# Optimization experiments

Measured on AMD Instinct MI355X. Metric: run time of the kernel, lower is better.

The kernel has to match this reference:

```python
import jax, jax.numpy as jnp
import numpy as np

N, D, H, E = 4096, 256, 8, 131072
HD = D // H
EPS = 1e-5


def layernorm(x, g, b):
    mu = jnp.mean(x, axis=-1, keepdims=True)
    var = jnp.mean((x - mu) ** 2, axis=-1, keepdims=True)
    return (x - mu) * jax.lax.rsqrt(var + EPS) * g + b


def setup_inputs() -> dict:
    key = jax.random.key(0)
    ks = jax.random.split(key, 20)
    s = 1.0 / np.sqrt(D)
    x = jax.random.normal(ks[0], (N, D), jnp.float32)
    adj = jax.random.uniform(ks[1], (N, N)) < 0.01
    adj_mask = adj | jnp.eye(N, dtype=bool)  # self-loops keep softmax rows finite
    edge_index = jax.random.randint(ks[2], (2, E), 0, N, dtype=jnp.int64)
    edge_attr = jax.random.normal(ks[3], (E, D), jnp.float32)
    p = {
        'wq': jax.random.normal(ks[4], (D, D)) * s, 'bq': jnp.zeros((D,)),
        'wk': jax.random.normal(ks[5], (D, D)) * s, 'bk': jnp.zeros((D,)),
        'wv': jax.random.normal(ks[6], (D, D)) * s, 'bv': jnp.zeros((D,)),
        'wo': jax.random.normal(ks[7], (D, D)) * s, 'bo': jnp.zeros((D,)),
        'we': jax.random.normal(ks[8], (D, H)) * s, 'be': jnp.zeros((H,)),
        'w1': jax.random.normal(ks[9], (D, 4 * D)) * s, 'b1': jnp.zeros((4 * D,)),
        'w2': jax.random.normal(ks[10], (4 * D, D)) * (1.0 / np.sqrt(4 * D)), 'b2': jnp.zeros((D,)),
        'g1': jnp.ones((D,)), 'beta1': jnp.zeros((D,)),
        'g2': jnp.ones((D,)), 'beta2': jnp.zeros((D,)),
    }
    return dict(x=x, adj_mask=adj_mask, edge_index=edge_index, edge_attr=edge_attr, **p)


def reference(x, adj_mask, edge_index, edge_attr, wq, bq, wk, bk, wv, bv, wo, bo,
              we, be, w1, b1, w2, b2, g1, beta1, g2, beta2):
    n = x.shape[0]
    Q = (x @ wq + bq).reshape(n, H, HD)
    K = (x @ wk + bk).reshape(n, H, HD)
    V = (x @ wv + bv).reshape(n, H, HD)
    scores = jnp.einsum('nhd,mhd->nmh', Q, K) / np.sqrt(HD)  # [N,N,H]
    edge_bias = edge_attr @ we + be                          # [E,H]
    scores = scores.at[edge_index[0], edge_index[1]].add(edge_bias)
    s = jnp.transpose(scores, (0, 2, 1))                     # [N,H,N]
    s = jnp.where(adj_mask[:, None, :], s, -jnp.inf)
    attn = jax.nn.softmax(s, axis=-1)                        # dropout eval-mode no-op
    ctx = jnp.einsum('nhm,mhd->nhd', attn, V).reshape(n, D)
    attn_out = ctx @ wo + bo
    x1 = layernorm(x + attn_out, g1, beta1)
    ff = jax.nn.gelu(x1 @ w1 + b1, approximate=False) @ w2 + b2
    return layernorm(x1 + ff, g2, beta2)
```

## Files before the change

### kernel.cpp

```cpp
#include <hip/hip_runtime.h>
#include <math.h>

#define NN   4096
#define DD   256
#define HH   8
#define HD   32
#define DFF  1024
#define QKVW 768
#define AC   128
#define EC   128
#define SCPAD 129
#define QSP  36
#define NPB  2

typedef unsigned short ushort_t;
typedef __attribute__((ext_vector_type(8))) short short8;
typedef __attribute__((ext_vector_type(4))) float f32x4;

__device__ __forceinline__ float bf2f(unsigned short u){
  union { unsigned int i; float f; } v; v.i = ((unsigned int)u) << 16; return v.f;
}
__device__ __forceinline__ unsigned short f2bf(float f){
  union { float f; unsigned int i; } v; v.f = f;
  unsigned int x = v.i;
  return (unsigned short)((x + 0x7FFFu + ((x >> 16) & 1u)) >> 16);
}
__device__ __forceinline__ float ldf(const void* p, size_t i, int isbf){
  return isbf ? bf2f(((const ushort_t*)p)[i]) : ((const float*)p)[i];
}
__device__ __forceinline__ ushort_t ldb16(const void* p, size_t i, int isbf){
  return isbf ? ((const ushort_t*)p)[i] : f2bf(((const float*)p)[i]);
}

__global__ void k_detect(const int* __restrict__ adj32, const int* __restrict__ ei32,
                         const unsigned int* __restrict__ g1w, int* __restrict__ flags,
                         int* __restrict__ counts, int* __restrict__ cursor){
  __shared__ int c0s, c1s;
  int t = threadIdx.x;
  if (t == 0) { c0s = 0; c1s = 0; }
  __syncthreads();
  int c0 = 0, c1 = 0;
  for (int i = t; i < 960; i += 256) if (adj32[(size_t)i * 4097] != 0) c0++;
  for (int i = t; i < 2048; i += 256) if (ei32[2*i + 1] != 0) c1++;
  atomicAdd(&c0s, c0); atomicAdd(&c1s, c1);
  for (int i = t; i < NN; i += 256) { counts[i] = 0; cursor[i] = 0; }
  __syncthreads();
  if (t == 0) {
    flags[0] = (c0s == 960) ? 1 : 0;
    flags[1] = (c1s > 100) ? 1 : 0;
    flags[2] = (g1w[0] == 0x3F803F80u) ? 1 : 0;
  }
}

#define NX    (NN * DD)
#define NWE   (DD * HH)
#define TPREP 768
#define NCSR  NN
__global__ __launch_bounds__(256) void k_prep(
    const void* __restrict__ adj, int* __restrict__ alist, int* __restrict__ acnt,
    const void* __restrict__ x, const void* __restrict__ wq, const void* __restrict__ wk,
    const void* __restrict__ wv, const void* __restrict__ wo, const void* __restrict__ w1,
    const void* __restrict__ w2, const void* __restrict__ we,
    const void* __restrict__ bq, const void* __restrict__ bk, const void* __restrict__ bv,
    const void* __restrict__ bo, const void* __restrict__ be, const void* __restrict__ b1,
    const void* __restrict__ b2, const void* __restrict__ g1, const void* __restrict__ be1,
    const void* __restrict__ g2, const void* __restrict__ be2,
    const int* __restrict__ ei, const int* __restrict__ flags,
    ushort_t* __restrict__ xb,
    ushort_t* __restrict__ wqkvT, ushort_t* __restrict__ woT,
    ushort_t* __restrict__ w1T, ushort_t* __restrict__ w2T,
    float* __restrict__ wef, float* __restrict__ bqkvf,
    float* __restrict__ bof, float* __restrict__ bef,
    float* __restrict__ b1f, float* __restrict__ b2f,
    float* __restrict__ g1f, float* __restrict__ be1f,
    float* __restrict__ g2f, float* __restrict__ be2f,
    int* __restrict__ counts, int E, int TOT)
{
  const int isbf = flags[2];
  const int t = threadIdx.x;
  if (blockIdx.x < NCSR) {
    __shared__ int cntS;
    __shared__ int actS[AC];
    const int n = blockIdx.x;
    if (t == 0) cntS = 0;
    __syncthreads();
    if (flags[0]) {
      const uint4* arow = (const uint4*)((const int*)adj + (size_t)n * NN);
      #pragma unroll
      for (int i = 0; i < 4; i++) {
        uint4 v = arow[t + 256 * i];
        int c0 = 4 * (t + 256 * i);
        if (v.x) { int p = atomicAdd(&cntS, 1); if (p < AC) actS[p] = c0; }
        if (v.y) { int p = atomicAdd(&cntS, 1); if (p < AC) actS[p] = c0 + 1; }
        if (v.z) { int p = atomicAdd(&cntS, 1); if (p < AC) actS[p] = c0 + 2; }
        if (v.w) { int p = atomicAdd(&cntS, 1); if (p < AC) actS[p] = c0 + 3; }
      }
    } else {
      const uint4* arow = (const uint4*)((const unsigned char*)adj + (size_t)n * NN);
      uint4 v = arow[t];
      unsigned int wsv[4] = {v.x, v.y, v.z, v.w};
      #pragma unroll
      for (int q = 0; q < 4; q++) {
        unsigned int u = wsv[q];
        int c0 = 16 * t + 4 * q;
        if (u & 0x000000FFu) { int p = atomicAdd(&cntS, 1); if (p < AC) actS[p] = c0; }
        if (u & 0x0000FF00u) { int p = atomicAdd(&cntS, 1); if (p < AC) actS[p] = c0 + 1; }
        if (u & 0x00FF0000u) { int p = atomicAdd(&cntS, 1); if (p < AC) actS[p] = c0 + 2; }
        if (u & 0xFF000000u) { int p = atomicAdd(&cntS, 1); if (p < AC) actS[p] = c0 + 3; }
      }
    }
    __syncthreads();
    int m = cntS; if (m > AC) m = AC;
    if (t == 0) acnt[n] = m;
    for (int j = t; j < m; j += 256) alist[(size_t)n * AC + j] = actS[j];
    return;
  }
  if (blockIdx.x < NCSR + TPREP) {
    __shared__ ushort_t tile[32][36];
    int b = blockIdx.x - NCSR;
    const void* src; ushort_t* dst; int R, C, ti;
    if (b < 64)       { src = wq; dst = wqkvT;              R = 256;  C = 256;  ti = b; }
    else if (b < 128) { src = wk; dst = wqkvT + 256 * 256;  R = 256;  C = 256;  ti = b - 64; }
    else if (b < 192) { src = wv; dst = wqkvT + 512 * 256;  R = 256;  C = 256;  ti = b - 128; }
    else if (b < 256) { src = wo; dst = woT;                R = 256;  C = 256;  ti = b - 192; }
    else if (b < 512) { src = w1; dst = w1T;                R = 256;  C = 1024; ti = b - 256; }
    else              { src = w2; dst = w2T;                R = 1024; C = 256;  ti = b - 512; }
    int tiles_c = C >> 5;
    int tr = ti / tiles_c, tc = ti - tr * tiles_c;
    int lr = t >> 3, lc0 = (t & 7) << 2;
    size_t sbase = (size_t)(tr * 32 + lr) * C + tc * 32 + lc0;
    if (isbf) {
      const ushort_t* s16 = (const ushort_t*)src + sbase;
      tile[lr][lc0+0] = s16[0]; tile[lr][lc0+1] = s16[1];
      tile[lr][lc0+2] = s16[2]; tile[lr][lc0+3] = s16[3];
    } else {
      const float4* sf = (const float4*)((const float*)src + sbase);
      float4 v = *sf;
      tile[lr][lc0+0] = f2bf(v.x); tile[lr][lc0+1] = f2bf(v.y);
      tile[lr][lc0+2] = f2bf(v.z); tile[lr][lc0+3] = f2bf(v.w);
    }
    __syncthreads();
    int i = t >> 3, j0 = (t & 7) << 2;
    ushort_t* dp = dst + (size_t)(tc * 32 + i) * R + tr * 32 + j0;
    ushort_t o0 = tile[j0][i], o1 = tile[j0+1][i], o2 = tile[j0+2][i], o3 = tile[j0+3][i];
    dp[0] = o0; dp[1] = o1; dp[2] = o2; dp[3] = o3;
    return;
  }
  const int ei32 = flags[1];
  const int stride = (gridDim.x - NCSR - TPREP) * 256;
  for (int i = (blockIdx.x - NCSR - TPREP) * 256 + t; i < TOT; i += stride) {
    int r = i;
    if (r < NX) { xb[r] = ldb16(x, r, isbf); continue; }
    r -= NX;
    if (r < E) {
      int src = ei32 ? ei[r] : ei[2 * r];
      if ((unsigned)src < (unsigned)NN) atomicAdd(&counts[src], 1);
      continue;
    }
    r -= E;
    if (r < NWE) { wef[r] = ldf(we, r, isbf); continue; }
    r -= NWE;
    if (r < QKVW) {
      const void* bs = (r < 256) ? bq : (r < 512) ? bk : bv;
      bqkvf[r] = ldf(bs, r & 255, isbf);
      continue;
    }
    r -= QKVW;
    if (r < DD)  { bof[r] = ldf(bo, r, isbf); continue; }   r -= DD;
    if (r < HH)  { bef[r] = ldf(be, r, isbf); continue; }   r -= HH;
    if (r < DFF) { b1f[r] = ldf(b1, r, isbf); continue; }   r -= DFF;
    if (r < DD)  { b2f[r] = ldf(b2, r, isbf); continue; }   r -= DD;
    if (r < DD)  { g1f[r] = ldf(g1, r, isbf); continue; }   r -= DD;
    if (r < DD)  { be1f[r] = ldf(be1, r, isbf); continue; } r -= DD;
    if (r < DD)  { g2f[r] = ldf(g2, r, isbf); continue; }   r -= DD;
    if (r < DD)  { be2f[r] = ldf(be2, r, isbf); }
  }
}

#define LDK 72
__global__ __launch_bounds__(256) void k_gemm(
    const ushort_t* __restrict__ A, const ushort_t* __restrict__ Bt,
    const float* __restrict__ bias, void* __restrict__ C,
    int M, int Nn, int K, int act, int mode,
    float* __restrict__ qf, ushort_t* __restrict__ kbuf, ushort_t* __restrict__ vbuf)
{
  __shared__ ushort_t As[64 * LDK];
  __shared__ ushort_t Bs[64 * LDK];
  const int t = threadIdx.x;
  const int wave = t >> 6, lane = t & 63;
  const int l15 = lane & 15, quad = lane >> 4;
  const int wr = wave >> 1, wc = wave & 1;
  const int bm0 = blockIdx.y * 64, bn0 = blockIdx.x * 64;

  const int arow = t >> 2, akg = (t & 3) << 4;

  f32x4 acc[2][2] = {};

  const ushort_t* ap = A  + (size_t)(bm0 + arow) * K + akg;
  const ushort_t* bp = Bt + (size_t)(bn0 + arow) * K + akg;
  uint4 a0 = *(const uint4*)ap;
  uint4 a1 = *(const uint4*)(ap + 8);
  uint4 b0 = *(const uint4*)bp;
  uint4 b1 = *(const uint4*)(bp + 8);

  for (int k0 = 0; k0 < K; k0 += 64) {
    __syncthreads();
    *(uint4*)(&As[arow * LDK + akg]) = a0;
    *(uint4*)(&As[arow * LDK + akg + 8]) = a1;
    *(uint4*)(&Bs[arow * LDK + akg]) = b0;
    *(uint4*)(&Bs[arow * LDK + akg + 8]) = b1;
    __syncthreads();
    if (k0 + 64 < K) {
      a0 = *(const uint4*)(ap + k0 + 64);
      a1 = *(const uint4*)(ap + k0 + 64 + 8);
      b0 = *(const uint4*)(bp + k0 + 64);
      b1 = *(const uint4*)(bp + k0 + 64 + 8);
    }
    #pragma unroll
    for (int kk = 0; kk < 2; kk++) {
      short8 af[2], bf[2];
      #pragma unroll
      for (int fr = 0; fr < 2; fr++)
        af[fr] = *(const short8*)(&As[(wr * 32 + fr * 16 + l15) * LDK + kk * 32 + quad * 8]);
      #pragma unroll
      for (int fc = 0; fc < 2; fc++)
        bf[fc] = *(const short8*)(&Bs[(wc * 32 + fc * 16 + l15) * LDK + kk * 32 + quad * 8]);
      #pragma unroll
      for (int fr = 0; fr < 2; fr++)
        #pragma unroll
        for (int fc = 0; fc < 2; fc++)
          acc[fr][fc] = __builtin_amdgcn_mfma_f32_16x16x32_bf16(af[fr], bf[fc], acc[fr][fc], 0, 0, 0);
    }
  }

  #pragma unroll
  for (int fr = 0; fr < 2; fr++) {
    #pragma unroll
    for (int fc = 0; fc < 2; fc++) {
      int gn = bn0 + wc * 32 + fc * 16 + l15;
      float bcol = bias[gn];
      #pragma unroll
      for (int r = 0; r < 4; r++) {
        int gm = bm0 + wr * 32 + fr * 16 + quad * 4 + r;
        float v = acc[fr][fc][r] + bcol;
        if (act) v = 0.5f * v * (1.0f + erff(v * 0.70710678118654752f));
        if (mode == 2) {
          if (gn < 256)      qf[(size_t)gm * 256 + gn] = v;
          else if (gn < 512) kbuf[(size_t)gm * 256 + (gn - 256)] = f2bf(v);
          else               vbuf[(size_t)gm * 256 + (gn - 512)] = f2bf(v);
        } else {
          ((ushort_t*)C)[(size_t)gm * Nn + gn] = f2bf(v);
        }
      }
    }
  }
}

__global__ __launch_bounds__(256) void k_mid(
    const ushort_t* __restrict__ A, const ushort_t* __restrict__ Bt,
    const float* __restrict__ bias,
    float* __restrict__ qf, ushort_t* __restrict__ kbuf, ushort_t* __restrict__ vbuf,
    const void* __restrict__ ea, const float* __restrict__ wef,
    const float* __restrict__ bef, float* __restrict__ sbias,
    int E, const int* __restrict__ flags,
    const int* __restrict__ ei, const int* __restrict__ off,
    int* __restrict__ cursor, int* __restrict__ sdst, int* __restrict__ seid)
{
  __shared__ __align__(16) char smem[64 * LDK * 2 * 2];
  const int t = threadIdx.x;
  if (blockIdx.x < 768) {
    ushort_t* As = (ushort_t*)smem;
    ushort_t* Bs = As + 64 * LDK;
    const int wave = t >> 6, lane = t & 63;
    const int l15 = lane & 15, quad = lane >> 4;
    const int wr = wave >> 1, wc = wave & 1;
    const int bn0 = (blockIdx.x % 12) * 64, bm0 = (blockIdx.x / 12) * 64;
    const int arow = t >> 2, akg = (t & 3) << 4;
    const int K = DD;

    f32x4 acc[2][2] = {};

    const ushort_t* ap = A  + (size_t)(bm0 + arow) * K + akg;
    const ushort_t* bp = Bt + (size_t)(bn0 + arow) * K + akg;
    uint4 a0 = *(const uint4*)ap;
    uint4 a1 = *(const uint4*)(ap + 8);
    uint4 b0 = *(const uint4*)bp;
    uint4 b1 = *(const uint4*)(bp + 8);

    for (int k0 = 0; k0 < K; k0 += 64) {
      __syncthreads();
      *(uint4*)(&As[arow * LDK + akg]) = a0;
      *(uint4*)(&As[arow * LDK + akg + 8]) = a1;
      *(uint4*)(&Bs[arow * LDK + akg]) = b0;
      *(uint4*)(&Bs[arow * LDK + akg + 8]) = b1;
      __syncthreads();
      if (k0 + 64 < K) {
        a0 = *(const uint4*)(ap + k0 + 64);
        a1 = *(const uint4*)(ap + k0 + 64 + 8);
        b0 = *(const uint4*)(bp + k0 + 64);
        b1 = *(const uint4*)(bp + k0 + 64 + 8);
      }
      #pragma unroll
      for (int kk = 0; kk < 2; kk++) {
        short8 af[2], bf[2];
        #pragma unroll
        for (int fr = 0; fr < 2; fr++)
          af[fr] = *(const short8*)(&As[(wr * 32 + fr * 16 + l15) * LDK + kk * 32 + quad * 8]);
        #pragma unroll
        for (int fc = 0; fc < 2; fc++)
          bf[fc] = *(const short8*)(&Bs[(wc * 32 + fc * 16 + l15) * LDK + kk * 32 + quad * 8]);
        #pragma unroll
        for (int fr = 0; fr < 2; fr++)
          #pragma unroll
          for (int fc = 0; fc < 2; fc++)
            acc[fr][fc] = __builtin_amdgcn_mfma_f32_16x16x32_bf16(af[fr], bf[fc], acc[fr][fc], 0, 0, 0);
      }
    }

    #pragma unroll
    for (int fr = 0; fr < 2; fr++) {
      #pragma unroll
      for (int fc = 0; fc < 2; fc++) {
        int gn = bn0 + wc * 32 + fc * 16 + l15;
        float bcol = bias[gn];
        #pragma unroll
        for (int r = 0; r < 4; r++) {
          int gm = bm0 + wr * 32 + fr * 16 + quad * 4 + r;
          float v = acc[fr][fc][r] + bcol;
          if (gn < 256)      qf[(size_t)gm * 256 + gn] = v;
          else if (gn < 512) kbuf[(size_t)gm * 256 + (gn - 256)] = f2bf(v);
          else               vbuf[(size_t)gm * 256 + (gn - 512)] = f2bf(v);
        }
      }
    }
    return;
  }
  float* wel = (float*)smem;
  const int b = blockIdx.x - 768;
  #pragma unroll
  for (int j = 0; j < 8; j++) wel[j * DD + t] = wef[t * 8 + j];
  const int isbf = flags[2];
  if (t < 32) {
    int i = b * 32 + t;
    if (i < E) {
      int src, dst;
      if (flags[1]) { src = ei[i];     dst = ei[E + i]; }
      else          { src = ei[2 * i]; dst = ei[2 * (E + i)]; }
      if ((unsigned)src < (unsigned)NN) {
        if ((unsigned)dst >= (unsigned)NN) dst = 0;
        int pos = off[src] + atomicAdd(&cursor[src], 1);
        sdst[pos] = dst; seid[pos] = i;
      }
    }
  }
  __syncthreads();
  int idx = b * 256 + t;
  int e = idx >> 3, p = idx & 7;
  float acc[8] = {};
  if (e < E) {
    if (isbf) {
      const uint4* base = (const uint4*)((const ushort_t*)ea + (size_t)e * DD);
      #pragma unroll
      for (int q = 0; q < 4; q++) {
        uint4 u = base[q * 8 + p];
        int dbase = 64 * q + 8 * p;
        float f[8];
        union { unsigned int i; float f; } cv;
        cv.i = u.x << 16; f[0] = cv.f; cv.i = u.x & 0xFFFF0000u; f[1] = cv.f;
        cv.i = u.y << 16; f[2] = cv.f; cv.i = u.y & 0xFFFF0000u; f[3] = cv.f;
        cv.i = u.z << 16; f[4] = cv.f; cv.i = u.z & 0xFFFF0000u; f[5] = cv.f;
        cv.i = u.w << 16; f[6] = cv.f; cv.i = u.w & 0xFFFF0000u; f[7] = cv.f;
        #pragma unroll
        for (int j = 0; j < 8; j++)
          #pragma unroll
          for (int h = 0; h < 8; h++)
            acc[h] = fmaf(f[j], wel[h * DD + dbase + j], acc[h]);
      }
    } else {
      const float4* base = (const float4*)((const float*)ea + (size_t)e * DD);
      #pragma unroll
      for (int q = 0; q < 8; q++) {
        float4 u = base[q * 8 + p];
        int dbase = 32 * q + 4 * p;
        #pragma unroll
        for (int h = 0; h < 8; h++) {
          acc[h] = fmaf(u.x, wel[h * DD + dbase + 0], acc[h]);
          acc[h] = fmaf(u.y, wel[h * DD + dbase + 1], acc[h]);
          acc[h] = fmaf(u.z, wel[h * DD + dbase + 2], acc[h]);
          acc[h] = fmaf(u.w, wel[h * DD + dbase + 3], acc[h]);
        }
      }
    }
  }
  #pragma unroll
  for (int h = 0; h < 8; h++) {
    acc[h] += __shfl_xor(acc[h], 1, 8);
    acc[h] += __shfl_xor(acc[h], 2, 8);
    acc[h] += __shfl_xor(acc[h], 4, 8);
  }
  if (e < E) sbias[(size_t)e * 8 + p] = acc[p] + bef[p];
}

__global__ __launch_bounds__(512) void k_gemmln(
    const ushort_t* __restrict__ A, const ushort_t* __restrict__ Bt,
    const float* __restrict__ bias, const void* __restrict__ res, int res_raw,
    void* __restrict__ outf, ushort_t* __restrict__ outb,
    const float* __restrict__ g, const float* __restrict__ beta,
    int final_mode, const int* __restrict__ flags, int K)
{
  __shared__ ushort_t As[16 * LDK];
  __shared__ ushort_t Bs[256 * LDK];
  __shared__ float p1[16][8];
  __shared__ float p2[16][8];
  const int t = threadIdx.x;
  const int wave = t >> 6, lane = t & 63;
  const int l15 = lane & 15, quad = lane >> 4;
  const int bm0 = blockIdx.x * 16;

  const int arow = t >> 3, akg = (t & 7) << 3;
  const int brow = t >> 1, bkg = (t & 1) << 5;

  f32x4 acc[2] = {};

  const ushort_t* ap = A + (size_t)(bm0 + arow) * K + akg;
  const ushort_t* bp = Bt + (size_t)brow * K + bkg;
  uint4 a0{};
  if (t < 128) a0 = *(const uint4*)ap;
  uint4 b0 = *(const uint4*)bp;
  uint4 b1 = *(const uint4*)(bp + 8);
  uint4 b2 = *(const uint4*)(bp + 16);
  uint4 b3 = *(const uint4*)(bp + 24);

  for (int k0 = 0; k0 < K; k0 += 64) {
    __syncthreads();
    if (t < 128) *(uint4*)(&As[arow * LDK + akg]) = a0;
    *(uint4*)(&Bs[brow * LDK + bkg])      = b0;
    *(uint4*)(&Bs[brow * LDK + bkg + 8])  = b1;
    *(uint4*)(&Bs[brow * LDK + bkg + 16]) = b2;
    *(uint4*)(&Bs[brow * LDK + bkg + 24]) = b3;
    __syncthreads();
    if (k0 + 64 < K) {
      if (t < 128) a0 = *(const uint4*)(ap + k0 + 64);
      b0 = *(const uint4*)(bp + k0 + 64);
      b1 = *(const uint4*)(bp + k0 + 64 + 8);
      b2 = *(const uint4*)(bp + k0 + 64 + 16);
      b3 = *(const uint4*)(bp + k0 + 64 + 24);
    }
    #pragma unroll
    for (int kk = 0; kk < 2; kk++) {
      short8 af  = *(const short8*)(&As[l15 * LDK + kk * 32 + quad * 8]);
      short8 bf0 = *(const short8*)(&Bs[(wave * 32 +      l15) * LDK + kk * 32 + quad * 8]);
      short8 bf1 = *(const short8*)(&Bs[(wave * 32 + 16 + l15) * LDK + kk * 32 + quad * 8]);
      acc[0] = __builtin_amdgcn_mfma_f32_16x16x32_bf16(af, bf0, acc[0], 0, 0, 0);
      acc[1] = __builtin_amdgcn_mfma_f32_16x16x32_bf16(af, bf1, acc[1], 0, 0, 0);
    }
  }

  const int isbf = flags[2];
  float v[2][4];
  #pragma unroll
  for (int fc = 0; fc < 2; fc++) {
    int gn = wave * 32 + fc * 16 + l15;
    float bc = bias[gn];
    #pragma unroll
    for (int r = 0; r < 4; r++) {
      int gm = bm0 + quad * 4 + r;
      float rv = res_raw ? ldf(res, (size_t)gm * DD + gn, isbf)
                         : ((const float*)res)[(size_t)gm * DD + gn];
      v[fc][r] = acc[fc][r] + bc + rv;
    }
  }
  float s1[4];
  #pragma unroll
  for (int r = 0; r < 4; r++) {
    s1[r] = v[0][r] + v[1][r];
    #pragma unroll
    for (int o = 1; o < 16; o <<= 1) s1[r] += __shfl_xor(s1[r], o, 64);
  }
  if (l15 == 0) {
    #pragma unroll
    for (int r = 0; r < 4; r++) p1[quad * 4 + r][wave] = s1[r];
  }
  __syncthreads();
  float mu[4];
  #pragma unroll
  for (int r = 0; r < 4; r++) {
    float m = 0.f;
    #pragma unroll
    for (int w = 0; w < 8; w++) m += p1[quad * 4 + r][w];
    mu[r] = m * (1.0f / 256.0f);
  }
  float s2[4];
  #pragma unroll
  for (int r = 0; r < 4; r++) {
    float d0 = v[0][r] - mu[r], d1 = v[1][r] - mu[r];
    s2[r] = d0 * d0 + d1 * d1;
    #pragma unroll
    for (int o = 1; o < 16; o <<= 1) s2[r] += __shfl_xor(s2[r], o, 64);
  }
  if (l15 == 0) {
    #pragma unroll
    for (int r = 0; r < 4; r++) p2[quad * 4 + r][wave] = s2[r];
  }
  __syncthreads();
  float rs[4];
  #pragma unroll
  for (int r = 0; r < 4; r++) {
    float q = 0.f;
    #pragma unroll
    for (int w = 0; w < 8; w++) q += p2[quad * 4 + r][w];
    rs[r] = rsqrtf(q * (1.0f / 256.0f) + 1e-5f);
  }
  #pragma unroll
  for (int fc = 0; fc < 2; fc++) {
    int gn = wave * 32 + fc * 16 + l15;
    float gv = g[gn], bv = beta[gn];
    #pragma unroll
    for (int r = 0; r < 4; r++) {
      int gm = bm0 + quad * 4 + r;
      float res_v = (v[fc][r] - mu[r]) * rs[r] * gv + bv;
      if (outb) {
        ((float*)outf)[(size_t)gm * DD + gn] = res_v;
        outb[(size_t)gm * DD + gn] = f2bf(res_v);
      } else {
        if (final_mode && isbf)
          ((ushort_t*)outf)[(size_t)gm * DD + gn] = f2bf(res_v);
        else
          ((float*)outf)[(size_t)gm * DD + gn] = res_v;
      }
    }
  }
}

__global__ __launch_bounds__(256) void k_scan(const int* __restrict__ counts,
                                              int* __restrict__ off){
  __shared__ int wsum[4];
  const int t = threadIdx.x, lid = t & 63, wid = t >> 6;
  int loc[16]; int s = 0;
  #pragma unroll
  for (int j = 0; j < 16; j++) { loc[j] = counts[t * 16 + j]; s += loc[j]; }
  const int tot = s;
  #pragma unroll
  for (int o = 1; o < 64; o <<= 1) {
    int u = __shfl_up(s, o, 64);
    if (lid >= o) s += u;
  }
  if (lid == 63) wsum[wid] = s;
  __syncthreads();
  int pre = 0;
  #pragma unroll
  for (int w = 0; w < 4; w++) if (w < wid) pre += wsum[w];
  int run = pre + s - tot;
  if (t == 0) off[0] = 0;
  #pragma unroll
  for (int j = 0; j < 16; j++) { run += loc[j]; off[t * 16 + j + 1] = run; }
}

__global__ __launch_bounds__(256) void k_attn(
    const float* __restrict__ qf, const ushort_t* __restrict__ kb,
    const ushort_t* __restrict__ vb,
    const int* __restrict__ alist, const int* __restrict__ acnt,
    const int* __restrict__ off, const int* __restrict__ sdst,
    const int* __restrict__ seid, const float* __restrict__ sbias,
    ushort_t* __restrict__ ctxb)
{
  __shared__ float qs[NPB][HH * QSP];
  __shared__ int   act[NPB][AC];
  __shared__ float sc[NPB][HH][SCPAD];
  __shared__ int   edst[NPB][EC];
  __shared__ float ivs[NPB][HH];

  const int t = threadIdx.x;
  const int n0 = blockIdx.x * NPB;

  int na[NPB], cn[NPB], st[NPB];
  #pragma unroll
  for (int s = 0; s < NPB; s++) {
    int n = n0 + s;
    qs[s][(t >> 5) * QSP + (t & 31)] = qf[(size_t)n * DD + t];
    na[s] = min(acnt[n], AC);
    st[s] = off[n];
    int c = off[n + 1] - st[s];
    cn[s] = c < 0 ? 0 : (c > EC ? EC : c);
    for (int j = t; j < na[s]; j += 256) act[s][j] = alist[(size_t)n * AC + j];
    for (int j = t; j < cn[s]; j += 256) edst[s][j] = sdst[st[s] + j];
  }
  __syncthreads();

  #pragma unroll
  for (int s = 0; s < NPB; s++) {
    for (int item = t; item < na[s] * HH; item += 256) {
      int idx = item >> 3, h = item & 7;
      int m = act[s][idx];
      const uint4* kr = (const uint4*)(kb + (size_t)m * DD + h * HD);
      const float* qh = qs[s] + h * QSP;
      float a = 0.f;
      #pragma unroll
      for (int q4 = 0; q4 < 4; q4++) {
        uint4 u = kr[q4];
        int b = q4 * 8;
        union { unsigned int i; float f; } cv;
        cv.i = u.x << 16;         a = fmaf(cv.f, qh[b+0], a);
        cv.i = u.x & 0xFFFF0000u; a = fmaf(cv.f, qh[b+1], a);
        cv.i = u.y << 16;         a = fmaf(cv.f, qh[b+2], a);
        cv.i = u.y & 0xFFFF0000u; a = fmaf(cv.f, qh[b+3], a);
        cv.i = u.z << 16;         a = fmaf(cv.f, qh[b+4], a);
        cv.i = u.z & 0xFFFF0000u; a = fmaf(cv.f, qh[b+5], a);
        cv.i = u.w << 16;         a = fmaf(cv.f, qh[b+6], a);
        cv.i = u.w & 0xFFFF0000u; a = fmaf(cv.f, qh[b+7], a);
      }
      sc[s][h][idx] = a * 0.17677669529663687f;
    }
  }
  __syncthreads();

  #pragma unroll
  for (int s = 0; s < NPB; s++) {
    for (int item = t; item < cn[s] * HH; item += 256) {
      int j = item >> 3, h = item & 7;
      int sid = seid[st[s] + j];
      int dst = edst[s][j];
      int pos = -1;
      for (int i = 0; i < na[s]; i++) if (act[s][i] == dst) { pos = i; break; }
      if (pos >= 0) atomicAdd(&sc[s][h][pos], sbias[(size_t)sid * 8 + h]);
    }
  }
  __syncthreads();

  #pragma unroll
  for (int s = 0; s < NPB; s++) {
    const int h = t >> 5, l = t & 31;
    float lm = -1e30f;
    for (int i = l; i < na[s]; i += 32) lm = fmaxf(lm, sc[s][h][i]);
    #pragma unroll
    for (int o = 16; o > 0; o >>= 1) lm = fmaxf(lm, __shfl_down(lm, o, 32));
    lm = __shfl(lm, 0, 32);
    float ls = 0.f;
    for (int i = l; i < na[s]; i += 32) {
      float e = __expf(sc[s][h][i] - lm);
      sc[s][h][i] = e;
      ls += e;
    }
    #pragma unroll
    for (int o = 16; o > 0; o >>= 1) ls += __shfl_down(ls, o, 32);
    if (l == 0) ivs[s][h] = 1.0f / ls;
  }
  __syncthreads();

  {
    const int s_ = t >> 7, h = (t >> 4) & 7, dp = t & 15;
    const int n_a = s_ ? na[1] : na[0];
    const ushort_t* vcol = vb + h * HD + 2 * dp;
    const float* scp = sc[s_][h];
    float a0 = 0.f, a1 = 0.f;
    int i = 0;
    for (; i + 8 <= n_a; i += 8) {
      int mm[8]; unsigned int vv[8];
      #pragma unroll
      for (int u = 0; u < 8; u++) mm[u] = act[s_][i + u];
      #pragma unroll
      for (int u = 0; u < 8; u++) vv[u] = *(const unsigned int*)(vcol + (size_t)mm[u] * DD);
      #pragma unroll
      for (int u = 0; u < 8; u++) {
        float p = scp[i + u];
        a0 = fmaf(p, bf2f((ushort_t)(vv[u] & 0xFFFFu)), a0);
        a1 = fmaf(p, bf2f((ushort_t)(vv[u] >> 16)), a1);
      }
    }
    for (; i < n_a; i++) {
      unsigned int v = *(const unsigned int*)(vcol + (size_t)act[s_][i] * DD);
      float p = scp[i];
      a0 = fmaf(p, bf2f((ushort_t)(v & 0xFFFFu)), a0);
      a1 = fmaf(p, bf2f((ushort_t)(v >> 16)), a1);
    }
    float iv = ivs[s_][h];
    unsigned int ob = ((unsigned int)f2bf(a1 * iv) << 16) | (unsigned int)f2bf(a0 * iv);
    *(unsigned int*)(ctxb + (size_t)(n0 + s_) * DD + h * HD + 2 * dp) = ob;
  }
}

extern "C" void kernel_launch(void* const* d_in, const int* in_sizes, int n_in,
                              void* d_out, int out_size, void* d_ws, size_t ws_size,
                              hipStream_t stream)
{
  const void* x   = d_in[0];
  const void* adj = d_in[1];
  const int*  ei  = (const int*)d_in[2];
  const void* ea  = d_in[3];
  const void* wq  = d_in[4];  const void* bq  = d_in[5];
  const void* wk  = d_in[6];  const void* bk  = d_in[7];
  const void* wv  = d_in[8];  const void* bv  = d_in[9];
  const void* wo  = d_in[10]; const void* bo  = d_in[11];
  const void* we  = d_in[12]; const void* be  = d_in[13];
  const void* w1  = d_in[14]; const void* b1  = d_in[15];
  const void* w2  = d_in[16]; const void* b2  = d_in[17];
  const void* g1  = d_in[18]; const void* be1 = d_in[19];
  const void* g2  = d_in[20]; const void* be2 = d_in[21];
  const int E = in_sizes[2] / 2;

  char* w = (char*)d_ws;
  size_t o = 0;
  auto carve = [&](size_t bytes) -> void* {
    void* p = w + o; o = (o + bytes + 255) & ~(size_t)255; return p;
  };
  ushort_t* xb    = (ushort_t*)carve((size_t)NN * DD * 2);
  float*    qfb   = (float*)   carve((size_t)NN * DD * 4);
  ushort_t* kbuf  = (ushort_t*)carve((size_t)NN * DD * 2);
  ushort_t* vbuf  = (ushort_t*)carve((size_t)NN * DD * 2);
  ushort_t* wqkvT = (ushort_t*)carve((size_t)QKVW * DD * 2);
  float*    bqkvf = (float*)   carve(QKVW * 4);
  ushort_t* woT   = (ushort_t*)carve((size_t)DD * DD * 2);
  ushort_t* w1T   = (ushort_t*)carve((size_t)DFF * DD * 2);
  ushort_t* w2T   = (ushort_t*)carve((size_t)DD * DFF * 2);
  float*    wef   = (float*)   carve((size_t)DD * HH * 4);
  float*    bof   = (float*)   carve(DD * 4);
  float*    bef   = (float*)   carve(HH * 4);
  float*    b1f   = (float*)   carve(DFF * 4);
  float*    b2f   = (float*)   carve(DD * 4);
  float*    g1f   = (float*)   carve(DD * 4);
  float*    be1f  = (float*)   carve(DD * 4);
  float*    g2f   = (float*)   carve(DD * 4);
  float*    be2f  = (float*)   carve(DD * 4);
  int*      counts = (int*)carve((size_t)NN * 4);
  int*      cursor = (int*)carve((size_t)NN * 4);
  int*      off    = (int*)carve((size_t)(NN + 1) * 4);
  int*      sdst   = (int*)carve((size_t)E * 4);
  int*      seid   = (int*)carve((size_t)E * 4);
  float*    sbias  = (float*)carve((size_t)E * HH * 4);
  int*      alist  = (int*)carve((size_t)NN * AC * 4);
  int*      acnt   = (int*)carve((size_t)NN * 4);
  ushort_t* ctxb     = (ushort_t*)carve((size_t)NN * DD * 2);
  float*    x1f      = (float*)   carve((size_t)NN * DD * 4);
  ushort_t* x1b      = (ushort_t*)carve((size_t)NN * DD * 2);
  ushort_t* hbufb    = (ushort_t*)carve((size_t)NN * DFF * 2);
  int*      flags    = (int*)carve(4 * 4);

  k_detect<<<1, 256, 0, stream>>>((const int*)adj, ei, (const unsigned int*)g1,
                                  flags, counts, cursor);

  const int TOT = NX + E + NWE + QKVW + DD + HH + DFF + DD + DD + DD + DD + DD;
  k_prep<<<NCSR + TPREP + 1280, 256, 0, stream>>>(
      adj, alist, acnt,
      x, wq, wk, wv, wo, w1, w2, we, bq, bk, bv, bo, be, b1, b2,
      g1, be1, g2, be2, ei, flags,
      xb, wqkvT, woT, w1T, w2T, wef, bqkvf,
      bof, bef, b1f, b2f, g1f, be1f, g2f, be2f, counts, E, TOT);

  k_scan<<<1, 256, 0, stream>>>(counts, off);

  int ebb = (E * 8 + 255) / 256;
  k_mid<<<768 + ebb, 256, 0, stream>>>(
      xb, wqkvT, bqkvf, qfb, kbuf, vbuf,
      ea, wef, bef, sbias, E, flags, ei, off, cursor, sdst, seid);

  k_attn<<<NN / NPB, 256, 0, stream>>>(qfb, kbuf, vbuf, alist, acnt, off, sdst,
                                       seid, sbias, ctxb);

  k_gemmln<<<NN / 16, 512, 0, stream>>>(
      ctxb, woT, bof, x, 1, x1f, x1b, g1f, be1f, 0, flags, DD);

  k_gemm<<<dim3(DFF / 64, NN / 64), 256, 0, stream>>>(
      x1b, w1T, b1f, hbufb, NN, DFF, DD, 1, 1, nullptr, nullptr, nullptr);

  k_gemmln<<<NN / 16, 512, 0, stream>>>(
      hbufb, w2T, b2f, x1f, 0, d_out, nullptr, g2f, be2f, 1, flags, DFF);
}
```

Measured before the change: 400.3 us.

## Precompute edge positions in CSR build, process four nodes per attention block

The linear search that maps each edge's destination to its slot in the node's active-neighbour list now runs once in the CSR-building stage of k_mid, which stores that slot index in place of the destination. k_attn reads the slot and edge id directly, so it no longer repeats the search for every head. k_attn also handles four nodes per block instead of two, and each thread accumulates four V columns with 64-bit loads instead of two with 32-bit loads. This adds a serial global-memory search per edge inside k_mid and more shared memory per attention block, which may reduce occupancy.

```diff
diff --git a/kernel.cpp b/kernel.cpp
--- a/kernel.cpp
+++ b/kernel.cpp
@@ -11,7 +11,7 @@
 #define EC   128
 #define SCPAD 129
 #define QSP  36
-#define NPB  2
+#define NPB  4
 
 typedef unsigned short ushort_t;
 typedef __attribute__((ext_vector_type(8))) short short8;
@@ -264,7 +264,8 @@
     const float* __restrict__ bef, float* __restrict__ sbias,
     int E, const int* __restrict__ flags,
     const int* __restrict__ ei, const int* __restrict__ off,
-    int* __restrict__ cursor, int* __restrict__ sdst, int* __restrict__ seid)
+    int* __restrict__ cursor, int* __restrict__ sdst, int* __restrict__ seid,
+    const int* __restrict__ alist, const int* __restrict__ acnt)
 {
   __shared__ __align__(16) char smem[64 * LDK * 2 * 2];
   const int t = threadIdx.x;
@@ -349,7 +350,11 @@
       if ((unsigned)src < (unsigned)NN) {
         if ((unsigned)dst >= (unsigned)NN) dst = 0;
         int pos = off[src] + atomicAdd(&cursor[src], 1);
-        sdst[pos] = dst; seid[pos] = i;
+        int na_s = min(acnt[src], AC);
+        const int* ap_ = alist + (size_t)src * AC;
+        int p = -1;
+        for (int q = 0; q < na_s; q++) if (ap_[q] == dst) { p = q; break; }
+        sdst[pos] = p; seid[pos] = i;
       }
     }
   }
@@ -560,14 +565,15 @@
     const float* __restrict__ qf, const ushort_t* __restrict__ kb,
     const ushort_t* __restrict__ vb,
     const int* __restrict__ alist, const int* __restrict__ acnt,
-    const int* __restrict__ off, const int* __restrict__ sdst,
+    const int* __restrict__ off, const int* __restrict__ spos,
     const int* __restrict__ seid, const float* __restrict__ sbias,
     ushort_t* __restrict__ ctxb)
 {
   __shared__ float qs[NPB][HH * QSP];
   __shared__ int   act[NPB][AC];
   __shared__ float sc[NPB][HH][SCPAD];
-  __shared__ int   edst[NPB][EC];
+  __shared__ int   eposS[NPB][EC];
+  __shared__ int   eidS[NPB][EC];
   __shared__ float ivs[NPB][HH];
 
   const int t = threadIdx.x;
@@ -583,7 +589,10 @@
     int c = off[n + 1] - st[s];
     cn[s] = c < 0 ? 0 : (c > EC ? EC : c);
     for (int j = t; j < na[s]; j += 256) act[s][j] = alist[(size_t)n * AC + j];
-    for (int j = t; j < cn[s]; j += 256) edst[s][j] = sdst[st[s] + j];
+    for (int j = t; j < cn[s]; j += 256) {
+      eposS[s][j] = spos[st[s] + j];
+      eidS[s][j]  = seid[st[s] + j];
+    }
   }
   __syncthreads();
 
@@ -618,11 +627,9 @@
   for (int s = 0; s < NPB; s++) {
     for (int item = t; item < cn[s] * HH; item += 256) {
       int j = item >> 3, h = item & 7;
-      int sid = seid[st[s] + j];
-      int dst = edst[s][j];
-      int pos = -1;
-      for (int i = 0; i < na[s]; i++) if (act[s][i] == dst) { pos = i; break; }
-      if (pos >= 0) atomicAdd(&sc[s][h][pos], sbias[(size_t)sid * 8 + h]);
+      int pos = eposS[s][j];
+      if (pos >= 0)
+        atomicAdd(&sc[s][h][pos], sbias[(size_t)eidS[s][j] * 8 + h]);
     }
   }
   __syncthreads();
@@ -648,34 +655,41 @@
   __syncthreads();
 
   {
-    const int s_ = t >> 7, h = (t >> 4) & 7, dp = t & 15;
-    const int n_a = s_ ? na[1] : na[0];
-    const ushort_t* vcol = vb + h * HD + 2 * dp;
+    const int s_ = t >> 6, h = (t >> 3) & 7, d4 = t & 7;
+    const int n_a = na[s_];
+    const ushort_t* vcol = vb + h * HD + 4 * d4;
     const float* scp = sc[s_][h];
-    float a0 = 0.f, a1 = 0.f;
+    float a0 = 0.f, a1 = 0.f, a2 = 0.f, a3 = 0.f;
     int i = 0;
     for (; i + 8 <= n_a; i += 8) {
-      int mm[8]; unsigned int vv[8];
+      int mm[8]; unsigned long long vv[8];
       #pragma unroll
       for (int u = 0; u < 8; u++) mm[u] = act[s_][i + u];
       #pragma unroll
-      for (int u = 0; u < 8; u++) vv[u] = *(const unsigned int*)(vcol + (size_t)mm[u] * DD);
+      for (int u = 0; u < 8; u++)
+        vv[u] = *(const unsigned long long*)(vcol + (size_t)mm[u] * DD);
       #pragma unroll
       for (int u = 0; u < 8; u++) {
         float p = scp[i + u];
         a0 = fmaf(p, bf2f((ushort_t)(vv[u] & 0xFFFFu)), a0);
-        a1 = fmaf(p, bf2f((ushort_t)(vv[u] >> 16)), a1);
+        a1 = fmaf(p, bf2f((ushort_t)((vv[u] >> 16) & 0xFFFFu)), a1);
+        a2 = fmaf(p, bf2f((ushort_t)((vv[u] >> 32) & 0xFFFFu)), a2);
+        a3 = fmaf(p, bf2f((ushort_t)(vv[u] >> 48)), a3);
       }
     }
     for (; i < n_a; i++) {
-      unsigned int v = *(const unsigned int*)(vcol + (size_t)act[s_][i] * DD);
+      unsigned long long v = *(const unsigned long long*)(vcol + (size_t)act[s_][i] * DD);
       float p = scp[i];
       a0 = fmaf(p, bf2f((ushort_t)(v & 0xFFFFu)), a0);
-      a1 = fmaf(p, bf2f((ushort_t)(v >> 16)), a1);
+      a1 = fmaf(p, bf2f((ushort_t)((v >> 16) & 0xFFFFu)), a1);
+      a2 = fmaf(p, bf2f((ushort_t)((v >> 32) & 0xFFFFu)), a2);
+      a3 = fmaf(p, bf2f((ushort_t)(v >> 48)), a3);
     }
     float iv = ivs[s_][h];
-    unsigned int ob = ((unsigned int)f2bf(a1 * iv) << 16) | (unsigned int)f2bf(a0 * iv);
-    *(unsigned int*)(ctxb + (size_t)(n0 + s_) * DD + h * HD + 2 * dp) = ob;
+    uint2 ob;
+    ob.x = ((unsigned int)f2bf(a1 * iv) << 16) | (unsigned int)f2bf(a0 * iv);
+    ob.y = ((unsigned int)f2bf(a3 * iv) << 16) | (unsigned int)f2bf(a2 * iv);
+    *(uint2*)(ctxb + (size_t)(n0 + s_) * DD + h * HD + 4 * d4) = ob;
   }
 }
 
@@ -751,7 +765,7 @@
   int ebb = (E * 8 + 255) / 256;
   k_mid<<<768 + ebb, 256, 0, stream>>>(
       xb, wqkvT, bqkvf, qfb, kbuf, vbuf,
-      ea, wef, bef, sbias, E, flags, ei, off, cursor, sdst, seid);
+      ea, wef, bef, sbias, E, flags, ei, off, cursor, sdst, seid, alist, acnt);
 
   k_attn<<<NN / NPB, 256, 0, stream>>>(qfb, kbuf, vbuf, alist, acnt, off, sdst,
                                        seid, sbias, ctxb);
```

After: 431.7 us. 7.8% more time.
